# Kernel optimization log

Measured on AMD Instinct MI355X. Metric: run time of the kernel, lower is better.

## Reference

```python
import jax, jax.numpy as jnp
import numpy as np

IN_F = 4096
OUT_F = 4096
RANK = 16
TOKENS = 8192
WORDS = IN_F // 16  # 16 int2 codes per int32 word
LORA_SCALE = 1.0


def pack_int2(codes):
    """codes: [out_f, in_f] int32 in {0,1,2} -> packed [out_f, in_f//16] int32.
    Little-endian: code k of a word sits at bits [2k, 2k+1]."""
    c = codes.reshape(codes.shape[0], -1, 16)  # [out, words, 16]
    shifts = jnp.arange(16, dtype=jnp.int32) * 2
    return jnp.sum(c << shifts, axis=-1).astype(jnp.int32)


def unpack_int2(packed, in_features):
    """packed: [out_f, words] int32 -> ternary floats [out_f, in_f] in {-1,0,+1}."""
    shifts = jnp.arange(16, dtype=jnp.int32) * 2
    codes = (packed[:, :, None] >> shifts) & 3  # [out, words, 16]
    codes = codes.reshape(packed.shape[0], -1)[:, :in_features]
    return codes - 1  # {0,1,2} -> {-1,0,+1}


def setup_inputs() -> dict:
    key = jax.random.key(0)
    kx, kc, ka, km, kb, kA, kB = jax.random.split(key, 7)
    x = jax.random.normal(kx, (TOKENS, IN_F), dtype=jnp.float32)
    codes = jax.random.randint(kc, (OUT_F, IN_F), 0, 3, dtype=jnp.int32)  # {0,1,2}
    int2_packed = pack_int2(codes)  # [OUT_F, WORDS]
    alpha = jax.random.uniform(ka, (OUT_F,), dtype=jnp.float32) * 0.1 + 0.01
    mu = jax.random.normal(km, (OUT_F,), dtype=jnp.float32) * 0.01
    bias = jax.random.normal(kb, (OUT_F,), dtype=jnp.float32) * 0.02
    lora_A = jax.random.normal(kA, (RANK, IN_F), dtype=jnp.float32) * 0.02
    lora_B = jax.random.normal(kB, (OUT_F, RANK), dtype=jnp.float32) * 0.02
    return {"x": x, "int2_packed": int2_packed, "alpha": alpha, "mu": mu,
            "bias": bias, "lora_A": lora_A, "lora_B": lora_B}


def reference(x, int2_packed, alpha, mu, bias, lora_A, lora_B):
    # Unpack ternary weight T in {-1,0,+1}: [OUT_F, IN_F]
    T = unpack_int2(int2_packed, IN_F).astype(x.dtype)
    # ternary matmul, per-row scale alpha
    out = jnp.einsum('ti,oi->to', x, T) * alpha[None, :]
    # asymmetric shift: mu_o * sum_i x_i
    out = out + mu[None, :] * jnp.sum(x, axis=-1, keepdims=True)
    # LoRA correction: scale * (x A^T) B^T
    lora_out = jnp.einsum('tr,or->to', jnp.einsum('ti,ri->tr', x, lora_A), lora_B)
    out = out + LORA_SCALE * lora_out
    return out + bias[None, :]
```

## Files before the change

kernel.cpp:

```cpp
#include <hip/hip_runtime.h>
#include <stdint.h>

#define IN_F   4096
#define OUT_F  4096
#define TOKENS 8192
#define RANK   16

#define BM 256
#define BN 256
#define BK 128
#define NT (IN_F / BK)

typedef unsigned short u16;
typedef __attribute__((ext_vector_type(8))) short bf16x8;
typedef __attribute__((ext_vector_type(4))) float f32x4;
typedef __attribute__((ext_vector_type(4))) int i32x4;

#define GLDS16(g, l) __builtin_amdgcn_global_load_lds( \
    (__attribute__((address_space(1))) void*)(g),      \
    (__attribute__((address_space(3))) void*)(l), 16, 0, 0)

#define MEMFENCE asm volatile("" ::: "memory")
#define BARRIER  do { MEMFENCE; __builtin_amdgcn_s_barrier(); MEMFENCE; } while (0)
#define VMCNT10  asm volatile("s_waitcnt vmcnt(10)" ::: "memory")
#define VMCNT12  asm volatile("s_waitcnt vmcnt(12)" ::: "memory")
#define VMCNT0   asm volatile("s_waitcnt vmcnt(0)" ::: "memory")

__device__ __forceinline__ int swz4(int row) { return (row & 3) ^ ((row >> 2) & 1); }

__device__ __forceinline__ u16 bf16bits(float f) {
    unsigned int u = __builtin_bit_cast(unsigned int, f);
    unsigned int lsb = (u >> 16) & 1u;
    u += 0x7fffu + lsb;
    return (u16)(u >> 16);
}

__device__ __forceinline__ unsigned int quant4(float a, float b, float c, float d, float inv) {
    int qa = __float2int_rn(a * inv); qa = max(-127, min(127, qa));
    int qb = __float2int_rn(b * inv); qb = max(-127, min(127, qb));
    int qc = __float2int_rn(c * inv); qc = max(-127, min(127, qc));
    int qd = __float2int_rn(d * inv); qd = max(-127, min(127, qd));
    return (qa & 255) | ((qb & 255) << 8) | ((qc & 255) << 16) | ((qd & 255) << 24);
}

__global__ __launch_bounds__(256) void k_prep(const float* __restrict__ X,
                                              const int* __restrict__ packed,
                                              const float* __restrict__ lA,
                                              const float* __restrict__ lB,
                                              signed char* __restrict__ Xq,
                                              float* __restrict__ sArr,
                                              float* __restrict__ SArr,
                                              signed char* __restrict__ Wq,
                                              u16* __restrict__ Bl,
                                              signed char* __restrict__ Aq,
                                              float* __restrict__ aScale) {
    __shared__ float rs[4], rm[4];
    const int b = blockIdx.x;
    const int tid = threadIdx.x;
    const int lane = tid & 63;
    const int wv = tid >> 6;

    if (b < TOKENS) {
        const int t = b;
        const float4* X4 = (const float4*)(X + (size_t)t * IN_F);
        float4 v[4];
#pragma unroll
        for (int j = 0; j < 4; j++) v[j] = X4[j * 256 + tid];

        float s = 0.f, m = 0.f;
#pragma unroll
        for (int j = 0; j < 4; j++) {
            s += v[j].x + v[j].y + v[j].z + v[j].w;
            m = fmaxf(m, fmaxf(fmaxf(fabsf(v[j].x), fabsf(v[j].y)),
                               fmaxf(fabsf(v[j].z), fabsf(v[j].w))));
        }
#pragma unroll
        for (int off = 32; off > 0; off >>= 1) {
            s += __shfl_down(s, off);
            m = fmaxf(m, __shfl_down(m, off));
        }
        if (lane == 0) { rs[wv] = s; rm[wv] = m; }
        __syncthreads();
        float S = rs[0] + rs[1] + rs[2] + rs[3];
        float M = fmaxf(fmaxf(rm[0], rm[1]), fmaxf(rm[2], rm[3]));
        M = fmaxf(M, 1e-20f);
        if (tid == 0) { SArr[t] = S; sArr[t] = M / 127.0f; }

        float inv = 127.0f / M;
        unsigned int* Xq32 = (unsigned int*)(Xq + (size_t)t * IN_F);
#pragma unroll
        for (int j = 0; j < 4; j++)
            Xq32[j * 256 + tid] = quant4(v[j].x, v[j].y, v[j].z, v[j].w, inv);
    } else if (b < TOKENS + OUT_F * (IN_F / 16) / 256) {
        int idx = (b - TOKENS) * 256 + tid;
        int p = packed[idx];
        uint4 o;
        unsigned int w[4];
#pragma unroll
        for (int g = 0; g < 4; g++) {
            unsigned int word = 0;
#pragma unroll
            for (int j = 0; j < 4; j++) {
                int k = g * 4 + j;
                int bb = ((p >> (2 * k)) & 3) - 1;
                word |= (unsigned int)(bb & 255) << (8 * j);
            }
            w[g] = word;
        }
        o.x = w[0]; o.y = w[1]; o.z = w[2]; o.w = w[3];
        *(uint4*)(Wq + (size_t)idx * 16) = o;
    } else if (b < TOKENS + OUT_F * (IN_F / 16) / 256 + OUT_F / 256) {
        int o = (b - TOKENS - OUT_F * (IN_F / 16) / 256) * 256 + tid;
        const float4* B4 = (const float4*)(lB + (size_t)o * RANK);
        float4 b0 = B4[0], b1 = B4[1], b2 = B4[2], b3 = B4[3];
        union { u16 u[32]; uint4 q[4]; } ob;
        ob.u[0] = bf16bits(b0.x); ob.u[1] = bf16bits(b0.y); ob.u[2] = bf16bits(b0.z); ob.u[3] = bf16bits(b0.w);
        ob.u[4] = bf16bits(b1.x); ob.u[5] = bf16bits(b1.y); ob.u[6] = bf16bits(b1.z); ob.u[7] = bf16bits(b1.w);
        ob.u[8] = bf16bits(b2.x); ob.u[9] = bf16bits(b2.y); ob.u[10] = bf16bits(b2.z); ob.u[11] = bf16bits(b2.w);
        ob.u[12] = bf16bits(b3.x); ob.u[13] = bf16bits(b3.y); ob.u[14] = bf16bits(b3.z); ob.u[15] = bf16bits(b3.w);
#pragma unroll
        for (int k = 16; k < 32; k++) ob.u[k] = 0;
        uint4* dst = (uint4*)(Bl + (size_t)o * 32);
        dst[0] = ob.q[0]; dst[1] = ob.q[1]; dst[2] = ob.q[2]; dst[3] = ob.q[3];
    } else {
        const int r = b - (TOKENS + OUT_F * (IN_F / 16) / 256 + OUT_F / 256);
        const float4* A4 = (const float4*)(lA + (size_t)r * IN_F);
        float4 v[4];
#pragma unroll
        for (int j = 0; j < 4; j++) v[j] = A4[j * 256 + tid];

        float m = 0.f;
#pragma unroll
        for (int j = 0; j < 4; j++)
            m = fmaxf(m, fmaxf(fmaxf(fabsf(v[j].x), fabsf(v[j].y)),
                               fmaxf(fabsf(v[j].z), fabsf(v[j].w))));
#pragma unroll
        for (int off = 32; off > 0; off >>= 1) m = fmaxf(m, __shfl_down(m, off));
        if (lane == 0) rm[wv] = m;
        __syncthreads();
        float M = fmaxf(fmaxf(rm[0], rm[1]), fmaxf(rm[2], rm[3]));
        M = fmaxf(M, 1e-20f);
        if (tid == 0) aScale[r] = M / 127.0f;

        float inv = 127.0f / M;
        unsigned int* Aq32 = (unsigned int*)(Aq + (size_t)r * IN_F);
#pragma unroll
        for (int j = 0; j < 4; j++)
            Aq32[j * 256 + tid] = quant4(v[j].x, v[j].y, v[j].z, v[j].w, inv);
    }
}

__global__ __launch_bounds__(256) void k_lora_y(const signed char* __restrict__ Xq,
                                                const signed char* __restrict__ Aq,
                                                const float* __restrict__ sArr,
                                                const float* __restrict__ aScale,
                                                u16* __restrict__ ypad) {
    __shared__ i32x4 red[4][64];
    const int tid = threadIdx.x;
    const int lane = tid & 63;
    const int wv = tid >> 6;
    const int t0 = blockIdx.x * 16;
    const int fr = lane & 15;
    const int q16 = (lane >> 4) * 16;

    i32x4 acc = {};
    const signed char* xrow = Xq + (size_t)(t0 + fr) * IN_F + wv * 1024 + q16;
    const signed char* arow = Aq + (size_t)fr * IN_F + wv * 1024 + q16;
#pragma unroll
    for (int k0 = 0; k0 < 1024; k0 += 64) {
        i32x4 af = *(const i32x4*)(xrow + k0);
        i32x4 bf = *(const i32x4*)(arow + k0);
        acc = __builtin_amdgcn_mfma_i32_16x16x64_i8(af, bf, acc, 0, 0, 0);
    }
    red[wv][lane] = acc;
    __syncthreads();
    if (wv == 0) {
        i32x4 s0 = red[0][lane], s1 = red[1][lane], s2 = red[2][lane], s3 = red[3][lane];
        const int c0 = lane & 15;
        const int r0 = (lane >> 4) * 4;
        float asc = aScale[c0];
#pragma unroll
        for (int r = 0; r < 4; r++) {
            int t = t0 + r0 + r;
            float y = sArr[t] * asc * (float)(s0[r] + s1[r] + s2[r] + s3[r]);
            ypad[(size_t)t * 32 + c0] = bf16bits(y);
            ypad[(size_t)t * 32 + 16 + c0] = 0;
        }
    }
}


#define STAGE_A(srcTile, h, dbuf)                                              \
    {                                                                          \
        _Pragma("unroll")                                                      \
        for (int j = 0; j < 2; j++) {                                          \
            int c = j * 512 + tid;                                             \
            int rho = c >> 3;                                                  \
            int sl = (c & 7) ^ (rho & 7);                                      \
            int trow = ((rho >> 6) << 7) + ((h) << 6) + (rho & 63);            \
            GLDS16(Xq + (size_t)(m0 + trow) * IN_F + (srcTile) * BK + sl * 16, \
                   smem + (dbuf) * 65536 + (h) * 16384 + j * 8192 + wvb);      \
        }                                                                      \
    }

#define STAGE_B(srcTile, h, dbuf)                                              \
    {                                                                          \
        _Pragma("unroll")                                                      \
        for (int j = 0; j < 2; j++) {                                          \
            int c = j * 512 + tid;                                             \
            int rho = c >> 3;                                                  \
            int sl = (c & 7) ^ (rho & 7);                                      \
            int tcol = ((rho >> 5) << 6) + ((h) << 5) + (rho & 31);            \
            GLDS16(Wq + (size_t)(n0 + tcol) * IN_F + (srcTile) * BK + sl * 16, \
                   smem + (dbuf) * 65536 + 32768 + (h) * 16384 + j * 8192 + wvb); \
        }                                                                      \
    }

#define READ_A(h)                                                              \
    {                                                                          \
        _Pragma("unroll")                                                      \
        for (int ml = 0; ml < 4; ml++) {                                       \
            _Pragma("unroll")                                                  \
            for (int ks = 0; ks < 2; ks++) {                                   \
                int rho = wmi * 64 + ml * 16 + fr;                             \
                int s = (ks * 4 + qs) ^ (rho & 7);                             \
                af[ml][ks] = *(const i32x4*)(smem + d * 65536 + (h) * 16384 +  \
                                             rho * 128 + s * 16);              \
            }                                                                  \
        }                                                                      \
    }

#define READ_B(hb)                                                             \
    {                                                                          \
        _Pragma("unroll")                                                      \
        for (int nl = 0; nl < 2; nl++) {                                       \
            _Pragma("unroll")                                                  \
            for (int ks = 0; ks < 2; ks++) {                                   \
                int rho = wni * 32 + nl * 16 + fr;                             \
                int s = (ks * 4 + qs) ^ (rho & 7);                             \
                bf[(hb) * 2 + nl][ks] = *(const i32x4*)(smem + d * 65536 +     \
                    32768 + (hb) * 16384 + rho * 128 + s * 16);                \
            }                                                                  \
        }                                                                      \
    }

#define MFMA_PHASE(ha, hb)                                                     \
    {                                                                          \
        __builtin_amdgcn_s_setprio(1);                                         \
        _Pragma("unroll")                                                      \
        for (int ml = 0; ml < 4; ml++) {                                       \
            _Pragma("unroll")                                                  \
            for (int nl = 0; nl < 2; nl++) {                                   \
                _Pragma("unroll")                                              \
                for (int ks = 0; ks < 2; ks++)                                 \
                    acc[(ha) * 4 + ml][(hb) * 2 + nl] =                        \
                        __builtin_amdgcn_mfma_i32_16x16x64_i8(                 \
                            af[ml][ks], bf[(hb) * 2 + nl][ks],                 \
                            acc[(ha) * 4 + ml][(hb) * 2 + nl], 0, 0, 0);       \
            }                                                                  \
        }                                                                      \
        __builtin_amdgcn_s_setprio(0);                                         \
    }

__global__ __launch_bounds__(512, 2) void k_gemm_i8(const signed char* __restrict__ Xq,
                                                    const signed char* __restrict__ Wq,
                                                    const float* __restrict__ sArr,
                                                    const float* __restrict__ SArr,
                                                    const float* __restrict__ alpha,
                                                    const float* __restrict__ mu,
                                                    const float* __restrict__ bias,
                                                    const u16* __restrict__ ypad,
                                                    const u16* __restrict__ Bl,
                                                    float* __restrict__ out) {
    __shared__ unsigned char smem[131072];

    const int tid = threadIdx.x;
    const int lane = tid & 63;
    const int wid = tid >> 6;
    const int wmi = wid >> 2;
    const int wni = wid & 3;
    const int fr = lane & 15;
    const int qs = lane >> 4;
    const int wvb = wid * 1024;

    int id = blockIdx.x;
    int swz = (id & 7) * 64 + (id >> 3);
    const int m0 = (swz >> 4) * BM;
    const int n0 = (swz & 15) * BN;

    i32x4 acc[8][4] = {};
    i32x4 af[4][2], bf[4][2];

    STAGE_A(0, 0, 0); STAGE_B(0, 0, 0); STAGE_B(0, 1, 0); STAGE_A(0, 1, 0);
    STAGE_A(1, 0, 1); STAGE_B(1, 0, 1); STAGE_B(1, 1, 1); STAGE_A(1, 1, 1);
    VMCNT12; BARRIER;

#pragma unroll 2
    for (int t = 0; t < NT; ++t) {
        const int d = t & 1;
        const int tp2 = (t + 2 < NT) ? (t + 2) : (NT - 1);
        READ_A(0); READ_B(0);
        VMCNT10; BARRIER;
        MFMA_PHASE(0, 0);
        BARRIER;
        READ_B(1);
        STAGE_A(tp2, 0, d);
        STAGE_B(tp2, 0, d);
        VMCNT12; BARRIER;
        MFMA_PHASE(0, 1);
        BARRIER;
        READ_A(1);
        STAGE_B(tp2, 1, d);
        BARRIER;
        MFMA_PHASE(1, 1);
        BARRIER;
        STAGE_A(tp2, 1, d);
        VMCNT12; BARRIER;
        MFMA_PHASE(1, 0);
        BARRIER;
    }

    VMCNT0; BARRIER;
#pragma unroll
    for (int j = 0; j < 2; j++) {
        int c = j * 512 + tid;
        int row = c >> 2;
        int sl = ((c & 3) ^ swz4(row)) << 4;
        GLDS16((const unsigned char*)ypad + (size_t)(m0 + row) * 64 + sl,
               smem + j * 8192 + wvb);
        GLDS16((const unsigned char*)Bl + (size_t)(n0 + row) * 64 + sl,
               smem + 16384 + j * 8192 + wvb);
    }

    const int r0 = qs * 4;
    const int c0 = fr;
    float av[4], mv[4], bv[4];
#pragma unroll
    for (int nt = 0; nt < 4; nt++) {
        int col = n0 + wni * 64 + nt * 16 + c0;
        av[nt] = alpha[col]; mv[nt] = mu[col]; bv[nt] = bias[col];
    }
    f32x4 facc[8][4];
#pragma unroll
    for (int mt = 0; mt < 8; mt++) {
        int rb = m0 + wmi * 128 + mt * 16 + r0;
        f32x4 sv = *(const f32x4*)(sArr + rb);
        f32x4 Sv = *(const f32x4*)(SArr + rb);
#pragma unroll
        for (int nt = 0; nt < 4; nt++)
#pragma unroll
            for (int r = 0; r < 4; r++)
                facc[mt][nt][r] = av[nt] * sv[r] * (float)acc[mt][nt][r] + fmaf(mv[nt], Sv[r], bv[nt]);
    }

    VMCNT0; BARRIER;
    bf16x8 yf[8], blf[4];
#pragma unroll
    for (int mt = 0; mt < 8; mt++) {
        int row = wmi * 128 + mt * 16 + fr;
        int s = (qs ^ swz4(row)) << 4;
        yf[mt] = *(const bf16x8*)(smem + row * 64 + s);
    }
#pragma unroll
    for (int nt = 0; nt < 4; nt++) {
        int row = wni * 64 + nt * 16 + fr;
        int s = (qs ^ swz4(row)) << 4;
        blf[nt] = *(const bf16x8*)(smem + 16384 + row * 64 + s);
    }
#pragma unroll
    for (int mt = 0; mt < 8; mt++)
#pragma unroll
        for (int nt = 0; nt < 4; nt++)
            facc[mt][nt] = __builtin_amdgcn_mfma_f32_16x16x32_bf16(yf[mt], blf[nt], facc[mt][nt], 0, 0, 0);

#pragma unroll
    for (int mt = 0; mt < 8; mt++) {
        int row = m0 + wmi * 128 + mt * 16 + r0;
#pragma unroll
        for (int nt = 0; nt < 4; nt++) {
            int col = n0 + wni * 64 + nt * 16 + c0;
            float* op = out + (size_t)row * OUT_F + col;
#pragma unroll
            for (int r = 0; r < 4; r++)
                op[(size_t)r * OUT_F] = facc[mt][nt][r];
        }
    }
}

extern "C" void kernel_launch(void* const* d_in, const int* in_sizes, int n_in,
                              void* d_out, int out_size, void* d_ws, size_t ws_size,
                              hipStream_t stream) {
    const float* x      = (const float*)d_in[0];
    const int*   packed = (const int*)d_in[1];
    const float* alpha  = (const float*)d_in[2];
    const float* mu     = (const float*)d_in[3];
    const float* bias   = (const float*)d_in[4];
    const float* lA     = (const float*)d_in[5];
    const float* lB     = (const float*)d_in[6];
    float* out = (float*)d_out;

    char* p = (char*)d_ws;
    signed char* Wq = (signed char*)p;             p += (size_t)OUT_F * IN_F;
    signed char* Xq = (signed char*)p;             p += (size_t)TOKENS * IN_F;
    float* sArr = (float*)p;                       p += (size_t)TOKENS * 4;
    float* SArr = (float*)p;                       p += (size_t)TOKENS * 4;
    u16* ypad = (u16*)p;                           p += (size_t)TOKENS * 32 * 2;
    u16* Bl = (u16*)p;                             p += (size_t)OUT_F * 32 * 2;
    signed char* Aq = (signed char*)p;             p += (size_t)RANK * IN_F;
    float* aScale = (float*)p;                     p += RANK * 4;

    const int prep_blocks = TOKENS + OUT_F * (IN_F / 16) / 256 + OUT_F / 256 + RANK;
    k_prep<<<dim3(prep_blocks), dim3(256), 0, stream>>>(x, packed, lA, lB, Xq, sArr, SArr, Wq, Bl, Aq, aScale);
    k_lora_y<<<dim3(TOKENS / 16), dim3(256), 0, stream>>>(Xq, Aq, sArr, aScale, ypad);

    k_gemm_i8<<<dim3(512), dim3(512), 0, stream>>>(Xq, Wq, sArr, SArr, alpha, mu, bias, ypad, Bl, out);
}
```

Measured before the change: 364.2 us.

## Rework int8 GEMM main loop into register-double-buffered one-tile-ahead pipeline

Restructures the K-loop of the int8 MFMA GEMM. Global-to-LDS staging now runs one tile ahead instead of two, and the first A/B fragments of the next tile are read from LDS into alternate register sets (afE/afO, bfP/bfQ) while the current tile's last MFMA quadrants still run. The aim is to hide LDS read latency behind MFMAs and to relax the vmcnt waits. The cost is more live fragment registers and a shallower global prefetch, which can expose HBM latency.

```diff
diff --git a/kernel.cpp b/kernel.cpp
--- a/kernel.cpp
+++ b/kernel.cpp
@@ -22,8 +22,8 @@
 
 #define MEMFENCE asm volatile("" ::: "memory")
 #define BARRIER  do { MEMFENCE; __builtin_amdgcn_s_barrier(); MEMFENCE; } while (0)
-#define VMCNT10  asm volatile("s_waitcnt vmcnt(10)" ::: "memory")
-#define VMCNT12  asm volatile("s_waitcnt vmcnt(12)" ::: "memory")
+#define VMCNT4   asm volatile("s_waitcnt vmcnt(4)" ::: "memory")
+#define VMCNT2   asm volatile("s_waitcnt vmcnt(2)" ::: "memory")
 #define VMCNT0   asm volatile("s_waitcnt vmcnt(0)" ::: "memory")
 
 __device__ __forceinline__ int swz4(int row) { return (row & 3) ^ ((row >> 2) & 1); }
@@ -216,7 +216,7 @@
         }                                                                      \
     }
 
-#define READ_A(h)                                                              \
+#define READ_Af(buf, h, dst)                                                   \
     {                                                                          \
         _Pragma("unroll")                                                      \
         for (int ml = 0; ml < 4; ml++) {                                       \
@@ -224,13 +224,13 @@
             for (int ks = 0; ks < 2; ks++) {                                   \
                 int rho = wmi * 64 + ml * 16 + fr;                             \
                 int s = (ks * 4 + qs) ^ (rho & 7);                             \
-                af[ml][ks] = *(const i32x4*)(smem + d * 65536 + (h) * 16384 +  \
-                                             rho * 128 + s * 16);              \
+                dst[ml][ks] = *(const i32x4*)(smem + (buf) * 65536 +           \
+                    (h) * 16384 + rho * 128 + s * 16);                         \
             }                                                                  \
         }                                                                      \
     }
 
-#define READ_B(hb)                                                             \
+#define READ_Bf(buf, h, dst)                                                   \
     {                                                                          \
         _Pragma("unroll")                                                      \
         for (int nl = 0; nl < 2; nl++) {                                       \
@@ -238,29 +238,51 @@
             for (int ks = 0; ks < 2; ks++) {                                   \
                 int rho = wni * 32 + nl * 16 + fr;                             \
                 int s = (ks * 4 + qs) ^ (rho & 7);                             \
-                bf[(hb) * 2 + nl][ks] = *(const i32x4*)(smem + d * 65536 +     \
-                    32768 + (hb) * 16384 + rho * 128 + s * 16);                \
+                dst[nl][ks] = *(const i32x4*)(smem + (buf) * 65536 +           \
+                    32768 + (h) * 16384 + rho * 128 + s * 16);                 \
             }                                                                  \
         }                                                                      \
     }
 
-#define MFMA_PHASE(ha, hb)                                                     \
+#define MFMA_Q(aset, bset, mtb, ntb)                                           \
     {                                                                          \
         __builtin_amdgcn_s_setprio(1);                                         \
         _Pragma("unroll")                                                      \
-        for (int ml = 0; ml < 4; ml++) {                                       \
+        for (int ml = 0; ml < 4; ml++)                                         \
             _Pragma("unroll")                                                  \
-            for (int nl = 0; nl < 2; nl++) {                                   \
+            for (int nl = 0; nl < 2; nl++)                                     \
                 _Pragma("unroll")                                              \
                 for (int ks = 0; ks < 2; ks++)                                 \
-                    acc[(ha) * 4 + ml][(hb) * 2 + nl] =                        \
+                    acc[(mtb) + ml][(ntb) + nl] =                              \
                         __builtin_amdgcn_mfma_i32_16x16x64_i8(                 \
-                            af[ml][ks], bf[(hb) * 2 + nl][ks],                 \
-                            acc[(ha) * 4 + ml][(hb) * 2 + nl], 0, 0, 0);       \
-            }                                                                  \
-        }                                                                      \
+                            aset[ml][ks], bset[nl][ks],                        \
+                            acc[(mtb) + ml][(ntb) + nl], 0, 0, 0);             \
         __builtin_amdgcn_s_setprio(0);                                         \
     }
+
+#define TILE_BODY(d, dn, tp1, BF0, BF1)                                        \
+                       \
+    READ_Bf(d, 1, BF1);                                                        \
+    STAGE_A(tp1, 0, dn); STAGE_B(tp1, 0, dn);                                  \
+    VMCNT4; BARRIER;                                                           \
+    MFMA_Q(afE, BF0, 0, 0);                                                    \
+    BARRIER;                                                                   \
+                       \
+    READ_Af(d, 1, afO);                                                        \
+    STAGE_B(tp1, 1, dn); STAGE_A(tp1, 1, dn);                                  \
+    VMCNT4; BARRIER;                                                           \
+    MFMA_Q(afE, BF1, 0, 2);                                                    \
+    BARRIER;                                                                   \
+                     \
+    READ_Af(dn, 0, afE);                                                       \
+    BARRIER;                                                                   \
+    MFMA_Q(afO, BF1, 4, 2);                                                    \
+    BARRIER;                                                                   \
+                     \
+    READ_Bf(dn, 0, BF1);                                                       \
+    VMCNT2; BARRIER;                                                           \
+    MFMA_Q(afO, BF0, 4, 0);                                                    \
+    BARRIER;
 
 __global__ __launch_bounds__(512, 2) void k_gemm_i8(const signed char* __restrict__ Xq,
                                                     const signed char* __restrict__ Wq,
@@ -289,35 +311,18 @@
     const int n0 = (swz & 15) * BN;
 
     i32x4 acc[8][4] = {};
-    i32x4 af[4][2], bf[4][2];
+    i32x4 afE[4][2], afO[4][2], bfP[2][2], bfQ[2][2];
 
     STAGE_A(0, 0, 0); STAGE_B(0, 0, 0); STAGE_B(0, 1, 0); STAGE_A(0, 1, 0);
-    STAGE_A(1, 0, 1); STAGE_B(1, 0, 1); STAGE_B(1, 1, 1); STAGE_A(1, 1, 1);
-    VMCNT12; BARRIER;
-
-#pragma unroll 2
-    for (int t = 0; t < NT; ++t) {
-        const int d = t & 1;
-        const int tp2 = (t + 2 < NT) ? (t + 2) : (NT - 1);
-        READ_A(0); READ_B(0);
-        VMCNT10; BARRIER;
-        MFMA_PHASE(0, 0);
-        BARRIER;
-        READ_B(1);
-        STAGE_A(tp2, 0, d);
-        STAGE_B(tp2, 0, d);
-        VMCNT12; BARRIER;
-        MFMA_PHASE(0, 1);
-        BARRIER;
-        READ_A(1);
-        STAGE_B(tp2, 1, d);
-        BARRIER;
-        MFMA_PHASE(1, 1);
-        BARRIER;
-        STAGE_A(tp2, 1, d);
-        VMCNT12; BARRIER;
-        MFMA_PHASE(1, 0);
-        BARRIER;
+    VMCNT4; BARRIER;
+    READ_Af(0, 0, afE); READ_Bf(0, 0, bfP);
+    VMCNT2; BARRIER;
+
+    for (int t = 0; t < NT; t += 2) {
+        const int ta = t + 1;
+        const int tb = (t + 2 < NT) ? (t + 2) : (NT - 1);
+        TILE_BODY(0, 1, ta, bfP, bfQ);
+        TILE_BODY(1, 0, tb, bfQ, bfP);
     }
 
     VMCNT0; BARRIER;
```

Measured after the change: 498.0 us. 1.37x slower.
